# Kernel tuning notes

Hardware: AMD Instinct MI355X
Metric: run time of the kernel (lower is better)

## Reference

```python
import jax, jax.numpy as jnp
import numpy as np

N_VOCAB = 267735
N_EMBED = 1024
CUTOFFS = [20000, 40000, 200000]
N_EMBEDS = [1024, 256, 64, 16]
STARTS = [0] + CUTOFFS
ENDS = CUTOFFS + [N_VOCAB]


def setup_inputs() -> dict:
    key = jax.random.key(0)
    ks = jax.random.split(key, 8)
    x = jax.random.randint(ks[0], (4, 8192), 0, N_VOCAB)
    inp = {"x": x}
    for i, (s, e, d) in enumerate(zip(STARTS, ENDS, N_EMBEDS)):
        # nn.init.normal_(weight, 0, 0.02)
        inp[f"table{i}"] = jax.random.normal(ks[1 + i], (e - s, d), jnp.float32) * 0.02
    for i, d in enumerate(N_EMBEDS[1:], start=1):
        # nn.Linear(d, N_EMBED, bias=False) weight, stored transposed as [d, N_EMBED]
        inp[f"proj{i}"] = jax.random.normal(ks[4 + i], (d, N_EMBED), jnp.float32) * (1.0 / np.sqrt(d))
    return inp


def reference(x, table0, table1, table2, table3, proj1, proj2, proj3):
    tables = [table0, table1, table2, table3]
    projs = [None, proj1, proj2, proj3]
    flat = x.reshape(-1)                                   # [N]
    emb = jnp.zeros((flat.shape[0], N_EMBED), jnp.float32)  # [N, n_embed]
    for i, (tab, s, e) in enumerate(zip(tables, STARTS, ENDS)):
        mask = (flat >= s) & (flat < e)                    # bucket membership
        local = jnp.clip(flat - s, 0, e - s - 1)           # in-range local ids
        ei = tab[local]                                    # [N, d_i] gather
        if i > 0:
            ei = ei @ projs[i]                             # project d_i -> n_embed
        emb = jnp.where(mask[:, None], ei, emb)            # scatter via select
    emb = emb * np.float32(np.sqrt(N_EMBED))
    return emb.reshape(*x.shape, N_EMBED)
```

## Files before the change

### kernel.cpp

```cpp
#include <hip/hip_runtime.h>

#define N_TOK    32768
#define NEMBED   1024
#define SCALE    32.0f
#define NTHREADS 512

#define G0 72
#define G1 80
#define G2 440
#define G3 176
#define GRID (G0 + G1 + G2 + G3)

typedef __attribute__((ext_vector_type(8))) short bf16x8;
typedef __attribute__((ext_vector_type(4))) float f32x4;

__device__ __forceinline__ int bucket_of(int idx) {
    return (idx < 20000) ? 0 : (idx < 40000) ? 1 : (idx < 200000) ? 2 : 3;
}

__device__ __forceinline__ unsigned pk(float a, float b) {
    return (__float_as_uint(a) >> 16) | (__float_as_uint(b) & 0xffff0000u);
}
union ABu { bf16x8 v; unsigned u[4]; };
__device__ __forceinline__ bf16x8 make_frag(const float* p) {
    float4 e0 = *(const float4*)p;
    float4 e1 = *(const float4*)(p + 4);
    ABu a;
    a.u[0] = pk(e0.x, e0.y); a.u[1] = pk(e0.z, e0.w);
    a.u[2] = pk(e1.x, e1.y); a.u[3] = pk(e1.z, e1.w);
    return a.v;
}
__device__ __forceinline__ bf16x8 zero_frag() {
    ABu a; a.u[0] = a.u[1] = a.u[2] = a.u[3] = 0u; return a.v;
}

__device__ __forceinline__ void store_tile(float* __restrict__ out,
                                           char* __restrict__ TBw,
                                           const f32x4* acc, int tok_a,
                                           int lane, int colbase) {
    int t = lane & 15, g = lane >> 4;
    int th0 = __shfl(tok_a, lane >> 3);
    int th1 = __shfl(tok_a, 8 + (lane >> 3));
    #pragma unroll
    for (int ch = 0; ch < 8; ++ch) {
        int nt0 = ch * 2;
        #pragma unroll
        for (int dnt = 0; dnt < 2; ++dnt) {
            f32x4 a = acc[nt0 + dnt];
            int i = dnt * 4 + g;
            f32x4 s;
            s[0] = a[0] * SCALE; s[1] = a[1] * SCALE;
            s[2] = a[2] * SCALE; s[3] = a[3] * SCALE;
            *(f32x4*)(TBw + ((t * 8 + (i ^ (t & 7))) << 4)) = s;
        }
        #pragma unroll
        for (int half = 0; half < 2; ++half) {
            int t2 = half * 8 + (lane >> 3);
            int tokd = half ? th1 : th0;
            f32x4 v = *(const f32x4*)(TBw + ((t2 * 8 + ((lane & 7) ^ (t2 & 7))) << 4));
            if (tokd >= 0)
                *(float4*)(out + (size_t)tokd * NEMBED + colbase + nt0 * 16 + (lane & 7) * 4)
                    = make_float4(v[0], v[1], v[2], v[3]);
        }
    }
}

__global__ void classify_kernel(const int* __restrict__ x,
                                int* __restrict__ cnt,
                                int* __restrict__ lists) {
    __shared__ int s_cnt[4], s_base[4];
    int tid = threadIdx.x;
    if (tid < 4) s_cnt[tid] = 0;
    __syncthreads();
    int t = blockIdx.x * blockDim.x + tid;
    int b = 0, p = 0;
    if (t < N_TOK) {
        b = bucket_of(x[t]);
        p = atomicAdd(&s_cnt[b], 1);
    }
    __syncthreads();
    if (tid < 4) s_base[tid] = atomicAdd(&cnt[tid], s_cnt[tid]);
    __syncthreads();
    if (t < N_TOK) lists[b * N_TOK + s_base[b] + p] = t;
}

__device__ __forceinline__ void run_copy(const int* __restrict__ x,
                                         const float* __restrict__ table0,
                                         const int* __restrict__ list0,
                                         float* __restrict__ out,
                                         int n, int wv0, int nwv) {
    int lane = threadIdx.x & 63;
    const float4* t4 = (const float4*)table0;
    float4* o4 = (float4*)out;
    #pragma unroll 1
    for (int i = wv0; i < n; i += nwv) {
        int tok = __builtin_amdgcn_readfirstlane(list0[i]);
        int row = __builtin_amdgcn_readfirstlane(x[tok]);
        #pragma unroll
        for (int q = 0; q < 4; ++q) {
            float4 v = t4[(size_t)row * 256 + q * 64 + lane];
            v.x *= SCALE; v.y *= SCALE; v.z *= SCALE; v.w *= SCALE;
            o4[(size_t)tok * 256 + q * 64 + lane] = v;
        }
    }
}

template <int D>
__device__ void run_proj_mfma(const int* __restrict__ x,
                              const float* __restrict__ table,
                              const float* __restrict__ proj,
                              const int* __restrict__ list_b,
                              float* __restrict__ out,
                              int n, int start, int cs,
                              int wj0, int wjs,
                              char* __restrict__ PL, char* __restrict__ TB) {
    constexpr int KS = (D + 31) / 32;
    int tid = threadIdx.x, lane = tid & 63;
    char* TBw = TB + (tid >> 6) * 2048;

    constexpr int ITEMS = KS * 2048;
    #pragma unroll 1
    for (int it = tid; it < ITEMS; it += NTHREADS) {
        int j0 = (it & 1) * 4;
        int ln = (it >> 1) & 63;
        int nt = (it >> 7) & 15;
        int ks = it >> 11;
        int kb = ks * 32 + ((ln >> 4) << 3) + j0;
        int col = cs * 256 + nt * 16 + (ln & 15);
        float f0 = (kb + 0 < D) ? proj[(size_t)(kb + 0) * NEMBED + col] : 0.f;
        float f1 = (kb + 1 < D) ? proj[(size_t)(kb + 1) * NEMBED + col] : 0.f;
        float f2 = (kb + 2 < D) ? proj[(size_t)(kb + 2) * NEMBED + col] : 0.f;
        float f3 = (kb + 3 < D) ? proj[(size_t)(kb + 3) * NEMBED + col] : 0.f;
        *(uint2*)(PL + (((ks * 16 + nt) * 64 + ln) << 4) + j0 * 2) =
            make_uint2(pk(f0, f1), pk(f2, f3));
    }
    __syncthreads();

    int nmt = (n + 15) >> 4;
    #pragma unroll 1
    for (int mt = wj0; mt < nmt; mt += wjs) {
        int ia = mt * 16 + (lane & 15);
        int tok_a = (ia < n) ? list_b[ia] : -1;
        int row_a = (tok_a >= 0) ? (x[tok_a] - start) : 0;
        const float* rp = table + (size_t)row_a * D;
        int k0 = (lane >> 4) << 3;
        bf16x8 e0 = (k0 < D) ? make_frag(rp + k0) : zero_frag();
        f32x4 acc[16];
        #pragma unroll
        for (int nt = 0; nt < 16; ++nt) acc[nt] = f32x4{0.f, 0.f, 0.f, 0.f};
        #pragma unroll
        for (int nt = 0; nt < 16; ++nt) {
            bf16x8 pf = *(const bf16x8*)(PL + ((nt * 64 + lane) << 4));
            acc[nt] = __builtin_amdgcn_mfma_f32_16x16x32_bf16(pf, e0, acc[nt], 0, 0, 0);
        }
        if constexpr (KS == 2) {
            bf16x8 e1 = make_frag(rp + 32 + k0);
            #pragma unroll
            for (int nt = 0; nt < 16; ++nt) {
                bf16x8 pf = *(const bf16x8*)(PL + (((16 + nt) * 64 + lane) << 4));
                acc[nt] = __builtin_amdgcn_mfma_f32_16x16x32_bf16(pf, e1, acc[nt], 0, 0, 0);
            }
        }
        store_tile(out, TBw, acc, tok_a, lane, cs * 256);
    }
}

__device__ void run_proj_mfma_big(const int* __restrict__ x,
                                  const float* __restrict__ table,
                                  const float* __restrict__ proj,
                                  const int* __restrict__ list_b,
                                  float* __restrict__ out,
                                  int n, int start, int cs,
                                  int c0, int cstr,
                                  char* __restrict__ PL, char* __restrict__ TB) {
    int tid = threadIdx.x, lane = tid & 63, w = tid >> 6;
    char* TBw = TB + w * 2048;
    int nch = (n + 127) >> 7;
    #pragma unroll 1
    for (int c = c0; c < nch; c += cstr) {
        int ia = c * 128 + w * 16 + (lane & 15);
        int tok_a = (ia < n) ? list_b[ia] : -1;
        int row_a = (tok_a >= 0) ? (x[tok_a] - start) : 0;
        const float* rp = table + (size_t)row_a * 256;
        f32x4 acc[16];
        #pragma unroll
        for (int nt = 0; nt < 16; ++nt) acc[nt] = f32x4{0.f, 0.f, 0.f, 0.f};

        #pragma unroll 1
        for (int piece = 0; piece < 4; ++piece) {
            __syncthreads();
            #pragma unroll 1
            for (int it = tid; it < 4096; it += NTHREADS) {
                int j0 = (it & 1) * 4;
                int ln = (it >> 1) & 63;
                int nt = (it >> 7) & 15;
                int ks = it >> 11;
                int kb = piece * 64 + ks * 32 + ((ln >> 4) << 3) + j0;
                int col = cs * 256 + nt * 16 + (ln & 15);
                float f0 = proj[(size_t)(kb + 0) * NEMBED + col];
                float f1 = proj[(size_t)(kb + 1) * NEMBED + col];
                float f2 = proj[(size_t)(kb + 2) * NEMBED + col];
                float f3 = proj[(size_t)(kb + 3) * NEMBED + col];
                *(uint2*)(PL + (((ks * 16 + nt) * 64 + ln) << 4) + j0 * 2) =
                    make_uint2(pk(f0, f1), pk(f2, f3));
            }
            __syncthreads();
            int k0 = (lane >> 4) << 3;
            bf16x8 e0 = make_frag(rp + piece * 64 + k0);
            bf16x8 e1 = make_frag(rp + piece * 64 + 32 + k0);
            #pragma unroll
            for (int nt = 0; nt < 16; ++nt) {
                bf16x8 pf = *(const bf16x8*)(PL + ((nt * 64 + lane) << 4));
                acc[nt] = __builtin_amdgcn_mfma_f32_16x16x32_bf16(pf, e0, acc[nt], 0, 0, 0);
            }
            #pragma unroll
            for (int nt = 0; nt < 16; ++nt) {
                bf16x8 pf = *(const bf16x8*)(PL + (((16 + nt) * 64 + lane) << 4));
                acc[nt] = __builtin_amdgcn_mfma_f32_16x16x32_bf16(pf, e1, acc[nt], 0, 0, 0);
            }
        }
        store_tile(out, TBw, acc, tok_a, lane, cs * 256);
    }
}

__global__ __launch_bounds__(NTHREADS, 4)
void fused_embed_kernel(const int* __restrict__ x,
                        const float* __restrict__ t0, const float* __restrict__ t1,
                        const float* __restrict__ t2, const float* __restrict__ t3,
                        const float* __restrict__ p1, const float* __restrict__ p2,
                        const float* __restrict__ p3,
                        const int* __restrict__ cnt,
                        const int* __restrict__ lists,
                        float* __restrict__ out) {
    __shared__ __align__(16) char SM[49152];
    char* PL = SM;
    char* TB = SM + 32768;
    int bid = blockIdx.x;
    int w = threadIdx.x >> 6;

    if (bid < G0) {
        run_copy(x, t0, lists, out, cnt[0], bid * 8 + w, G0 * 8);
    } else if (bid < G0 + G1) {
        int lb = bid - G0;
        run_proj_mfma_big(x, t1, p1, lists + 1 * N_TOK, out, cnt[1], 20000,
                          lb & 3, lb >> 2, G1 / 4, PL, TB);
    } else if (bid < G0 + G1 + G2) {
        int lb = bid - (G0 + G1);
        run_proj_mfma<64>(x, t2, p2, lists + 2 * N_TOK, out, cnt[2], 40000,
                          lb & 3, (lb >> 2) * 8 + w, (G2 / 4) * 8, PL, TB);
    } else {
        int lb = bid - (G0 + G1 + G2);
        run_proj_mfma<16>(x, t3, p3, lists + 3 * N_TOK, out, cnt[3], 200000,
                          lb & 3, (lb >> 2) * 8 + w, (G3 / 4) * 8, PL, TB);
    }
}

extern "C" void kernel_launch(void* const* d_in, const int* in_sizes, int n_in,
                              void* d_out, int out_size, void* d_ws, size_t ws_size,
                              hipStream_t stream) {
    const int*   x  = (const int*)d_in[0];
    const float* t0 = (const float*)d_in[1];
    const float* t1 = (const float*)d_in[2];
    const float* t2 = (const float*)d_in[3];
    const float* t3 = (const float*)d_in[4];
    const float* p1 = (const float*)d_in[5];
    const float* p2 = (const float*)d_in[6];
    const float* p3 = (const float*)d_in[7];
    float* out = (float*)d_out;

    int* cnt   = (int*)d_ws;
    int* lists = cnt + 64;

    hipMemsetAsync(d_ws, 0, 64 * sizeof(int), stream);
    classify_kernel<<<N_TOK / 256, 256, 0, stream>>>(x, cnt, lists);

    fused_embed_kernel<<<GRID, NTHREADS, 0, stream>>>(x, t0, t1, t2, t3, p1, p2, p3,
                                                      cnt, lists, out);
}
```

Measured before the change: 45.83 us.

## Replace static work striding with dynamic atomic work queues per bucket

The copy path and the three projection paths no longer use fixed per-wave or per-block strides. Each wave, or each whole block for the large-K path, now claims its next row pair, M-tile or chunk from global atomic counters kept in the workspace, with one counter per bucket and column slice. The aim is to balance load across the statically partitioned grid, since bucket sizes vary with the input. The cost is an atomic round trip per work item, contention on shared counters, and extra block barriers in the big path. It also relies on those counters being zeroed before every launch.

```diff
diff --git a/kernel.cpp b/kernel.cpp
--- a/kernel.cpp
+++ b/kernel.cpp
@@ -17,6 +17,7 @@
 __device__ __forceinline__ int bucket_of(int idx) {
     return (idx < 20000) ? 0 : (idx < 40000) ? 1 : (idx < 200000) ? 2 : 3;
 }
+__device__ __forceinline__ int rfl(int v) { return __builtin_amdgcn_readfirstlane(v); }
 
 __device__ __forceinline__ unsigned pk(float a, float b) {
     return (__float_as_uint(a) >> 16) | (__float_as_uint(b) & 0xffff0000u);
@@ -88,19 +89,28 @@
                                          const float* __restrict__ table0,
                                          const int* __restrict__ list0,
                                          float* __restrict__ out,
-                                         int n, int wv0, int nwv) {
+                                         int n, int* __restrict__ q) {
     int lane = threadIdx.x & 63;
     const float4* t4 = (const float4*)table0;
     float4* o4 = (float4*)out;
-    #pragma unroll 1
-    for (int i = wv0; i < n; i += nwv) {
-        int tok = __builtin_amdgcn_readfirstlane(list0[i]);
-        int row = __builtin_amdgcn_readfirstlane(x[tok]);
-        #pragma unroll
-        for (int q = 0; q < 4; ++q) {
-            float4 v = t4[(size_t)row * 256 + q * 64 + lane];
-            v.x *= SCALE; v.y *= SCALE; v.z *= SCALE; v.w *= SCALE;
-            o4[(size_t)tok * 256 + q * 64 + lane] = v;
+    for (;;) {
+        int i0 = 0;
+        if (lane == 0) i0 = atomicAdd(q, 2);
+        i0 = rfl(i0);
+        if (i0 >= n) break;
+        #pragma unroll
+        for (int d = 0; d < 2; ++d) {
+            int i = i0 + d;
+            if (i < n) {
+                int tok = rfl(list0[i]);
+                int row = rfl(x[tok]);
+                #pragma unroll
+                for (int qq = 0; qq < 4; ++qq) {
+                    float4 v = t4[(size_t)row * 256 + qq * 64 + lane];
+                    v.x *= SCALE; v.y *= SCALE; v.z *= SCALE; v.w *= SCALE;
+                    o4[(size_t)tok * 256 + qq * 64 + lane] = v;
+                }
+            }
         }
     }
 }
@@ -112,7 +122,7 @@
                               const int* __restrict__ list_b,
                               float* __restrict__ out,
                               int n, int start, int cs,
-                              int wj0, int wjs,
+                              int* __restrict__ q,
                               char* __restrict__ PL, char* __restrict__ TB) {
     constexpr int KS = (D + 31) / 32;
     int tid = threadIdx.x, lane = tid & 63;
@@ -137,8 +147,12 @@
     __syncthreads();
 
     int nmt = (n + 15) >> 4;
-    #pragma unroll 1
-    for (int mt = wj0; mt < nmt; mt += wjs) {
+    for (;;) {
+        int mt = 0;
+        if (lane == 0) mt = atomicAdd(q, 1);
+        mt = rfl(mt);
+        if (mt >= nmt) break;
+
         int ia = mt * 16 + (lane & 15);
         int tok_a = (ia < n) ? list_b[ia] : -1;
         int row_a = (tok_a >= 0) ? (x[tok_a] - start) : 0;
@@ -171,13 +185,18 @@
                                   const int* __restrict__ list_b,
                                   float* __restrict__ out,
                                   int n, int start, int cs,
-                                  int c0, int cstr,
+                                  int* __restrict__ q, int* __restrict__ s_chunk,
                                   char* __restrict__ PL, char* __restrict__ TB) {
     int tid = threadIdx.x, lane = tid & 63, w = tid >> 6;
     char* TBw = TB + w * 2048;
     int nch = (n + 127) >> 7;
-    #pragma unroll 1
-    for (int c = c0; c < nch; c += cstr) {
+    for (;;) {
+        if (tid == 0) *s_chunk = atomicAdd(q, 1);
+        __syncthreads();
+        int c = *s_chunk;
+        __syncthreads();
+        if (c >= nch) break;
+
         int ia = c * 128 + w * 16 + (lane & 15);
         int tok_a = (ia < n) ? list_b[ia] : -1;
         int row_a = (tok_a >= 0) ? (x[tok_a] - start) : 0;
@@ -229,29 +248,30 @@
                         const float* __restrict__ t2, const float* __restrict__ t3,
                         const float* __restrict__ p1, const float* __restrict__ p2,
                         const float* __restrict__ p3,
-                        const int* __restrict__ cnt,
+                        int* __restrict__ cnt,
                         const int* __restrict__ lists,
                         float* __restrict__ out) {
     __shared__ __align__(16) char SM[49152];
+    __shared__ int s_chunk;
     char* PL = SM;
     char* TB = SM + 32768;
+    int* Q = cnt + 8;
     int bid = blockIdx.x;
-    int w = threadIdx.x >> 6;
 
     if (bid < G0) {
-        run_copy(x, t0, lists, out, cnt[0], bid * 8 + w, G0 * 8);
+        run_copy(x, t0, lists, out, cnt[0], Q + 12);
     } else if (bid < G0 + G1) {
         int lb = bid - G0;
         run_proj_mfma_big(x, t1, p1, lists + 1 * N_TOK, out, cnt[1], 20000,
-                          lb & 3, lb >> 2, G1 / 4, PL, TB);
+                          lb & 3, Q + 8 + (lb & 3), &s_chunk, PL, TB);
     } else if (bid < G0 + G1 + G2) {
         int lb = bid - (G0 + G1);
         run_proj_mfma<64>(x, t2, p2, lists + 2 * N_TOK, out, cnt[2], 40000,
-                          lb & 3, (lb >> 2) * 8 + w, (G2 / 4) * 8, PL, TB);
+                          lb & 3, Q + 0 + (lb & 3), PL, TB);
     } else {
         int lb = bid - (G0 + G1 + G2);
         run_proj_mfma<16>(x, t3, p3, lists + 3 * N_TOK, out, cnt[3], 200000,
-                          lb & 3, (lb >> 2) * 8 + w, (G3 / 4) * 8, PL, TB);
+                          lb & 3, Q + 4 + (lb & 3), PL, TB);
     }
 }
 
```

Result: slower. 178.9 us (+290.3%).
